# Performance work log

Measured on AMD Instinct MI355X. Metric: run time of the kernel, lower is better.

Reference implementation:

```python
import jax, jax.numpy as jnp
import numpy as np

N_LAGS = 64
EPS = 1e-8


def setup_inputs() -> dict:
    key = jax.random.key(0)
    x = jax.random.normal(key, (16, 8, 250, 1024), dtype=jnp.float32)
    return {"x": x}


def reference(x):
    B, M, T, L = x.shape
    # rfft over all mics once (shared across pairs)
    X = jnp.fft.rfft(x, axis=-1)  # [B, M, T, L//2+1] complex
    # all mic pairs (m1 < m2), row-major order matching the torch double loop
    i1, i2 = np.triu_indices(M, k=1)
    X1 = X[:, i1]  # [B, P, T, F]
    X2 = X[:, i2]  # [B, P, T, F]
    R = X1 * jnp.conj(X2)
    R = R / (jnp.abs(R) + EPS)  # PHAT weighting
    cc = jnp.fft.irfft(R, n=L, axis=-1)        # [B, P, T, L]
    cc = jnp.fft.fftshift(cc, axes=-1)
    center = L // 2
    start = center - N_LAGS // 2
    return cc[..., start:start + N_LAGS]        # [B, P, T, n_lags]
```

## Files before the change

### kernel.cpp

```cpp
#include <hip/hip_runtime.h>
#include <math.h>

#define B_    16
#define M_    8
#define T_    250
#define L_    1024
#define NPAIR 28

#define KTOT   1024
#define CH_K   256
#define APITCH 264
#define NKT    8
#define NCHUNK 4
#define ZPITCH 1056

typedef _Float16 half8  __attribute__((ext_vector_type(8)));
typedef _Float16 half2t __attribute__((ext_vector_type(2)));
typedef float    floatx4 __attribute__((ext_vector_type(4)));

__device__ __align__(16) _Float16 g_Btw[64 * KTOT];

__constant__ int c_i1[NPAIR] = {0,0,0,0,0,0,0,1,1,1,1,1,1,2,2,2,2,2,3,3,3,3,4,4,4,5,5,6};
__constant__ int c_i2[NPAIR] = {1,2,3,4,5,6,7,2,3,4,5,6,7,3,4,5,6,7,4,5,6,7,5,6,7,6,7,7};

__global__ void init_btw() {
    int idx = blockIdx.x * 256 + threadIdx.x;
    int n = idx >> 10, k = idx & 1023;
    float v;
    if (k == 0)      v = 1.0f / 1024.0f;
    else if (k == 1) v = (n & 1) ? (-1.0f / 1024.0f) : (1.0f / 1024.0f);
    else {
        int bin = k >> 1, tau = n - 32;
        int r = (tau * bin) & 1023;
        float ang = (float)r * (6.283185307179586f / 1024.0f);
        float s, c; sincosf(ang, &s, &c);
        v = ((k & 1) ? -s : c) * (2.0f / 1024.0f);
    }
    g_Btw[idx] = (_Float16)v;
}

#define SWZ(i) ((i) + ((i) >> 5))

__device__ inline float2 cmul(float2 a, float2 b) {
    return make_float2(fmaf(a.x, b.x, -a.y * b.y), fmaf(a.x, b.y, a.y * b.x));
}
__device__ inline float2 cadd(float2 a, float2 b) { return make_float2(a.x + b.x, a.y + b.y); }
__device__ inline float2 csub(float2 a, float2 b) { return make_float2(a.x - b.x, a.y - b.y); }
__device__ inline float2 cmni(float2 a) { return make_float2(a.y, -a.x); }

__device__ inline void dft8(float2 v[8]) {
    const float rt = 0.70710678118654752440f;
    float2 b0 = cadd(v[0], v[4]), b1 = cadd(v[1], v[5]);
    float2 b2 = cadd(v[2], v[6]), b3 = cadd(v[3], v[7]);
    float2 c0 = csub(v[0], v[4]);
    float2 t1 = csub(v[1], v[5]);
    float2 c1 = make_float2(rt * (t1.x + t1.y), rt * (t1.y - t1.x));
    float2 c2 = cmni(csub(v[2], v[6]));
    float2 t3 = csub(v[3], v[7]);
    float2 c3 = make_float2(rt * (t3.y - t3.x), -rt * (t3.x + t3.y));
    float2 f0 = cadd(b0, b2), f1 = cadd(b1, b3);
    float2 g0 = csub(b0, b2), g1 = cmni(csub(b1, b3));
    v[0] = cadd(f0, f1); v[4] = csub(f0, f1);
    v[2] = cadd(g0, g1); v[6] = csub(g0, g1);
    f0 = cadd(c0, c2); f1 = cadd(c1, c3);
    g0 = csub(c0, c2); g1 = cmni(csub(c1, c3));
    v[1] = cadd(f0, f1); v[5] = csub(f0, f1);
    v[3] = cadd(g0, g1); v[7] = csub(g0, g1);
}

__device__ inline void twiddle8(float2 v[8], float2 w1) {
    float2 w = w1;
    v[1] = cmul(v[1], w);
#pragma unroll
    for (int k = 2; k < 8; ++k) { w = cmul(w, w1); v[k] = cmul(v[k], w); }
}

__device__ inline int posmap(int k) {
    return ((k & 1) << 9) | (((k >> 1) & 7) << 6) | (((k >> 4) & 7) << 3) | ((k >> 7) & 7);
}

__global__ __launch_bounds__(512, 4) void gcc_main(const float* __restrict__ x,
                                                   float* __restrict__ out) {
    __shared__ float2 s_z[4 * ZPITCH];
    __shared__ __align__(16) union {
        float2   lut[512];
        _Float16 A[32 * APITCH];
    } su;

    const int tid = threadIdx.x;
    const int t = blockIdx.x, b = blockIdx.y;
    const int f = tid & 127, c = tid >> 7;
    float2* Zb = s_z + c * ZPITCH;

    {
        float s, cv, ang = (float)tid * (-6.283185307179586f / 1024.0f);
        sincosf(ang, &s, &cv);
        su.lut[tid] = make_float2(cv, s);
    }

    const float* xa = x + (((size_t)b * M_ + 2 * c) * T_ + t) * L_;
    const float* xb = xa + (size_t)T_ * L_;
#pragma unroll
    for (int e = 0; e < 2; ++e) {
        float4 va = *(const float4*)(xa + f * 8 + e * 4);
        float4 vb = *(const float4*)(xb + f * 8 + e * 4);
        int i = f * 8 + e * 4;
        Zb[SWZ(i + 0)] = make_float2(va.x, vb.x);
        Zb[SWZ(i + 1)] = make_float2(va.y, vb.y);
        Zb[SWZ(i + 2)] = make_float2(va.z, vb.z);
        Zb[SWZ(i + 3)] = make_float2(va.w, vb.w);
    }
    __syncthreads();

#pragma unroll
    for (int q = 0; q < 4; ++q) {
        int u = f + 128 * q;
        float2 a = Zb[SWZ(u)], d = Zb[SWZ(u + 512)];
        Zb[SWZ(u)]       = cadd(a, d);
        Zb[SWZ(u + 512)] = cmul(csub(a, d), su.lut[u]);
    }
    __syncthreads();

    {
        const int base = (f >> 6) * 512 + (f & 63);
        float2 v[8];
#pragma unroll
        for (int r = 0; r < 8; ++r) v[r] = Zb[SWZ(base + 64 * r)];
        dft8(v);
        twiddle8(v, su.lut[2 * (f & 63)]);
#pragma unroll
        for (int k = 0; k < 8; ++k) Zb[SWZ(base + 64 * k)] = v[k];
    }
    __syncthreads();

    {
        const int base = (f >> 3) * 64 + (f & 7);
        float2 v[8];
#pragma unroll
        for (int r = 0; r < 8; ++r) v[r] = Zb[SWZ(base + 8 * r)];
        dft8(v);
        twiddle8(v, su.lut[16 * (f & 7)]);
#pragma unroll
        for (int k = 0; k < 8; ++k) Zb[SWZ(base + 8 * k)] = v[k];
    }
    __syncthreads();

    {
        const int base = f * 8;
        float2 v[8];
#pragma unroll
        for (int r = 0; r < 8; ++r) v[r] = Zb[SWZ(base + r)];
        dft8(v);
#pragma unroll
        for (int k = 0; k < 8; ++k) Zb[SWZ(base + k)] = v[k];
    }
    __syncthreads();

    const int lane = tid & 63, wv = tid >> 6;
    const int mt = wv >> 2, nt = wv & 3;
    const int l15 = lane & 15, quad = lane >> 4;
    const int arow = mt * 16 + l15;
    const _Float16* Bbase = g_Btw + (nt * 16 + l15) * KTOT;
    floatx4 acc = {0.0f, 0.0f, 0.0f, 0.0f};

    const int bl = tid & 127, pg = tid >> 7;

#define PAIRA(p_, a_, b_)                                                     \
    {                                                                         \
        float2 X1 = Xs[a_], X2 = Xs[b_];                                      \
        float rr = X1.x * X2.x + X1.y * X2.y;                                 \
        float ri = X1.y * X2.x - X1.x * X2.y;                                 \
        float m2 = rr * rr + ri * ri;                                         \
        float inv = (m2 > 1e-30f) ? rsqrtf(m2) : 0.0f;                        \
        *(half2t*)&su.A[(p_) * APITCH + 2 * bl] =                             \
            (half2t){(_Float16)(rr * inv), (_Float16)(ri * inv)};             \
    }

    auto fillA = [&](int h) {
        const int beta = h * 128 + bl;
        const int pa = posmap(beta);
        const int pb = posmap((1024 - beta) & 1023);
        float2 Xs[8];
#pragma unroll
        for (int cc = 0; cc < 4; ++cc) {
            float2 Aa = s_z[cc * ZPITCH + SWZ(pa)];
            float2 Bb = s_z[cc * ZPITCH + SWZ(pb)];
            Xs[2 * cc]     = make_float2(0.5f * (Aa.x + Bb.x), 0.5f * (Aa.y - Bb.y));
            Xs[2 * cc + 1] = make_float2(0.5f * (Aa.y + Bb.y), 0.5f * (Bb.x - Aa.x));
        }
        if (pg == 0) {
            PAIRA(0, 0, 1) PAIRA(1, 0, 2) PAIRA(2, 0, 3) PAIRA(3, 0, 4)
            PAIRA(4, 0, 5) PAIRA(5, 0, 6) PAIRA(6, 0, 7)
        } else if (pg == 1) {
            PAIRA(7, 1, 2) PAIRA(8, 1, 3) PAIRA(9, 1, 4) PAIRA(10, 1, 5)
            PAIRA(11, 1, 6) PAIRA(12, 1, 7) PAIRA(13, 2, 3)
        } else if (pg == 2) {
            PAIRA(14, 2, 4) PAIRA(15, 2, 5) PAIRA(16, 2, 6) PAIRA(17, 2, 7)
            PAIRA(18, 3, 4) PAIRA(19, 3, 5) PAIRA(20, 3, 6)
        } else {
            PAIRA(21, 3, 7) PAIRA(22, 4, 5) PAIRA(23, 4, 6) PAIRA(24, 4, 7)
            PAIRA(25, 5, 6) PAIRA(26, 5, 7) PAIRA(27, 6, 7)
        }
        if (h == 0 && bl == 0) {
#pragma unroll
            for (int pp = 0; pp < 7; ++pp) {
                const int p = pg * 7 + pp;
                const int pN = posmap(512);
                float2 Za = s_z[(c_i1[p] >> 1) * ZPITCH + SWZ(pN)];
                float2 Zc = s_z[(c_i2[p] >> 1) * ZPITCH + SWZ(pN)];
                float x1 = (c_i1[p] & 1) ? Za.y : Za.x;
                float x2 = (c_i2[p] & 1) ? Zc.y : Zc.x;
                float rr = x1 * x2;
                float inv = (rr * rr > 1e-30f) ? rsqrtf(rr * rr) : 0.0f;
                su.A[p * APITCH + 1] = (_Float16)(rr * inv);
            }
        }
    };

    for (int h = 0; h < NCHUNK; ++h) {
        fillA(h);
        __syncthreads();

        const _Float16* Ap = su.A + arow * APITCH;
        const _Float16* Bp = Bbase + h * CH_K;
#pragma unroll
        for (int kt = 0; kt < NKT; ++kt) {
            half8 af = *(const half8*)(Ap + kt * 32 + quad * 8);
            half8 bf = *(const half8*)(Bp + kt * 32 + quad * 8);
            acc = __builtin_amdgcn_mfma_f32_16x16x32_f16(af, bf, acc, 0, 0, 0);
        }
        __syncthreads();
    }

#pragma unroll
    for (int r = 0; r < 4; ++r) {
        int pair = mt * 16 + quad * 4 + r;
        if (pair < NPAIR)
            out[((((size_t)b * NPAIR + pair) * T_ + t) << 6) + nt * 16 + l15] = acc[r];
    }
}

extern "C" void kernel_launch(void* const* d_in, const int* in_sizes, int n_in,
                              void* d_out, int out_size, void* d_ws, size_t ws_size,
                              hipStream_t stream) {
    (void)in_sizes; (void)n_in; (void)d_ws; (void)ws_size; (void)out_size;
    hipLaunchKernelGGL(init_btw, dim3(256), dim3(256), 0, stream);
    hipLaunchKernelGGL(gcc_main, dim3(T_, B_), dim3(512), 0, stream,
                       (const float*)d_in[0], (float*)d_out);
}
```

Measured before the change: 294.8 us.

## Cut LDS footprint with XOR swizzles, register twiddles, smaller A chunks

Replaces padded shared-memory layouts with XOR-swizzled unpadded ones and drops the twiddle lookup table, computing twiddles with sincosf in registers instead. The A staging buffer shrinks to 128-wide chunks (8 chunks of 4 MFMAs), and the pair-normalisation work is redistributed over all 8 waves. The first FFT stage is fused with the global load, using strided coalesced reads. Together these reduce LDS use so launch bounds can request 8 blocks per CU, at the cost of twice as many barriers in the MFMA loop and extra trig work per thread.

```diff
diff --git a/kernel.cpp b/kernel.cpp
--- a/kernel.cpp
+++ b/kernel.cpp
@@ -8,11 +8,9 @@
 #define NPAIR 28
 
 #define KTOT   1024
-#define CH_K   256
-#define APITCH 264
-#define NKT    8
-#define NCHUNK 4
-#define ZPITCH 1056
+#define CH_K   128
+#define NKT    4
+#define NCHUNK 8
 
 typedef _Float16 half8  __attribute__((ext_vector_type(8)));
 typedef _Float16 half2t __attribute__((ext_vector_type(2)));
@@ -39,7 +37,8 @@
     g_Btw[idx] = (_Float16)v;
 }
 
-#define SWZ(i) ((i) + ((i) >> 5))
+#define PHI(i) ((i) ^ (((i) >> 4) & 15) ^ ((((i) >> 8) & 3) << 1))
+#define AXR(p) (8 * ((p) & 7))
 
 __device__ inline float2 cmul(float2 a, float2 b) {
     return make_float2(fmaf(a.x, b.x, -a.y * b.y), fmaf(a.x, b.y, a.y * b.x));
@@ -79,69 +78,70 @@
     return ((k & 1) << 9) | (((k >> 1) & 7) << 6) | (((k >> 4) & 7) << 3) | ((k >> 7) & 7);
 }
 
-__global__ __launch_bounds__(512, 4) void gcc_main(const float* __restrict__ x,
+__global__ __launch_bounds__(512, 8) void gcc_main(const float* __restrict__ x,
                                                    float* __restrict__ out) {
-    __shared__ float2 s_z[4 * ZPITCH];
-    __shared__ __align__(16) union {
-        float2   lut[512];
-        _Float16 A[32 * APITCH];
-    } su;
+    __shared__ float2 s_z[4 * 1024];
+    __shared__ __align__(16) _Float16 sA[32 * CH_K];
 
     const int tid = threadIdx.x;
     const int t = blockIdx.x, b = blockIdx.y;
     const int f = tid & 127, c = tid >> 7;
-    float2* Zb = s_z + c * ZPITCH;
-
-    {
-        float s, cv, ang = (float)tid * (-6.283185307179586f / 1024.0f);
-        sincosf(ang, &s, &cv);
-        su.lut[tid] = make_float2(cv, s);
-    }
-
-    const float* xa = x + (((size_t)b * M_ + 2 * c) * T_ + t) * L_;
-    const float* xb = xa + (size_t)T_ * L_;
-#pragma unroll
-    for (int e = 0; e < 2; ++e) {
-        float4 va = *(const float4*)(xa + f * 8 + e * 4);
-        float4 vb = *(const float4*)(xb + f * 8 + e * 4);
-        int i = f * 8 + e * 4;
-        Zb[SWZ(i + 0)] = make_float2(va.x, vb.x);
-        Zb[SWZ(i + 1)] = make_float2(va.y, vb.y);
-        Zb[SWZ(i + 2)] = make_float2(va.z, vb.z);
-        Zb[SWZ(i + 3)] = make_float2(va.w, vb.w);
-    }
-    __syncthreads();
-
-#pragma unroll
-    for (int q = 0; q < 4; ++q) {
-        int u = f + 128 * q;
-        float2 a = Zb[SWZ(u)], d = Zb[SWZ(u + 512)];
-        Zb[SWZ(u)]       = cadd(a, d);
-        Zb[SWZ(u + 512)] = cmul(csub(a, d), su.lut[u]);
-    }
-    __syncthreads();
-
-    {
+    float2* Zb = s_z + c * 1024;
+
+    float ws, wc;
+    sincosf((float)f * (-6.283185307179586f / 1024.0f), &ws, &wc);
+    const float2 w = make_float2(wc, ws);
+
+    {
+        const float* xa = x + (((size_t)b * M_ + 2 * c) * T_ + t) * L_;
+        const float* xb = xa + (size_t)T_ * L_;
+        float va[8], vb[8];
+#pragma unroll
+        for (int j = 0; j < 8; ++j) { va[j] = xa[f + 128 * j]; vb[j] = xb[f + 128 * j]; }
+        const float rt = 0.70710678118654752440f;
+#pragma unroll
+        for (int q = 0; q < 4; ++q) {
+            float2 a = make_float2(va[q], vb[q]);
+            float2 d = make_float2(va[q + 4], vb[q + 4]);
+            float2 tq = cmul(csub(a, d), w);
+            float2 r;
+            if (q == 0)      r = tq;
+            else if (q == 1) r = make_float2(rt * (tq.x + tq.y), rt * (tq.y - tq.x));
+            else if (q == 2) r = make_float2(tq.y, -tq.x);
+            else             r = make_float2(rt * (tq.y - tq.x), -rt * (tq.x + tq.y));
+            Zb[PHI(f + 128 * q)]       = cadd(a, d);
+            Zb[PHI(f + 128 * q + 512)] = r;
+        }
+    }
+    __syncthreads();
+
+    {
+        float2 wl = w;
+        if (f & 64) wl = cmul(wl, make_float2(0.92387953251128674f, 0.38268343236508977f));
+        const float2 wB = cmul(wl, wl);
         const int base = (f >> 6) * 512 + (f & 63);
         float2 v[8];
 #pragma unroll
-        for (int r = 0; r < 8; ++r) v[r] = Zb[SWZ(base + 64 * r)];
+        for (int r = 0; r < 8; ++r) v[r] = Zb[PHI(base + 64 * r)];
         dft8(v);
-        twiddle8(v, su.lut[2 * (f & 63)]);
-#pragma unroll
-        for (int k = 0; k < 8; ++k) Zb[SWZ(base + 64 * k)] = v[k];
-    }
-    __syncthreads();
-
-    {
+        twiddle8(v, wB);
+#pragma unroll
+        for (int k = 0; k < 8; ++k) Zb[PHI(base + 64 * k)] = v[k];
+    }
+    __syncthreads();
+
+    {
+        float s2, c2;
+        sincosf((float)(f & 7) * (-6.283185307179586f / 64.0f), &s2, &c2);
+        const float2 wC = make_float2(c2, s2);
         const int base = (f >> 3) * 64 + (f & 7);
         float2 v[8];
 #pragma unroll
-        for (int r = 0; r < 8; ++r) v[r] = Zb[SWZ(base + 8 * r)];
+        for (int r = 0; r < 8; ++r) v[r] = Zb[PHI(base + 8 * r)];
         dft8(v);
-        twiddle8(v, su.lut[16 * (f & 7)]);
-#pragma unroll
-        for (int k = 0; k < 8; ++k) Zb[SWZ(base + 8 * k)] = v[k];
+        twiddle8(v, wC);
+#pragma unroll
+        for (int k = 0; k < 8; ++k) Zb[PHI(base + 8 * k)] = v[k];
     }
     __syncthreads();
 
@@ -149,10 +149,10 @@
         const int base = f * 8;
         float2 v[8];
 #pragma unroll
-        for (int r = 0; r < 8; ++r) v[r] = Zb[SWZ(base + r)];
+        for (int r = 0; r < 8; ++r) v[r] = Zb[PHI(base + r)];
         dft8(v);
 #pragma unroll
-        for (int k = 0; k < 8; ++k) Zb[SWZ(base + k)] = v[k];
+        for (int k = 0; k < 8; ++k) Zb[PHI(base + k)] = v[k];
     }
     __syncthreads();
 
@@ -163,7 +163,10 @@
     const _Float16* Bbase = g_Btw + (nt * 16 + l15) * KTOT;
     floatx4 acc = {0.0f, 0.0f, 0.0f, 0.0f};
 
-    const int bl = tid & 127, pg = tid >> 7;
+    const int bl = lane;
+    const int pg = wv;
+
+    if (tid < 256) ((unsigned int*)sA)[1792 + tid] = 0u;
 
 #define PAIRA(p_, a_, b_)                                                     \
     {                                                                         \
@@ -172,47 +175,53 @@
         float ri = X1.y * X2.x - X1.x * X2.y;                                 \
         float m2 = rr * rr + ri * ri;                                         \
         float inv = (m2 > 1e-30f) ? rsqrtf(m2) : 0.0f;                        \
-        *(half2t*)&su.A[(p_) * APITCH + 2 * bl] =                             \
+        *(half2t*)&sA[(p_) * CH_K + ((2 * bl) ^ AXR(p_))] =                   \
             (half2t){(_Float16)(rr * inv), (_Float16)(ri * inv)};             \
     }
 
     auto fillA = [&](int h) {
-        const int beta = h * 128 + bl;
+        const int beta = h * 64 + bl;
         const int pa = posmap(beta);
         const int pb = posmap((1024 - beta) & 1023);
         float2 Xs[8];
 #pragma unroll
         for (int cc = 0; cc < 4; ++cc) {
-            float2 Aa = s_z[cc * ZPITCH + SWZ(pa)];
-            float2 Bb = s_z[cc * ZPITCH + SWZ(pb)];
+            float2 Aa = s_z[cc * 1024 + PHI(pa)];
+            float2 Bb = s_z[cc * 1024 + PHI(pb)];
             Xs[2 * cc]     = make_float2(0.5f * (Aa.x + Bb.x), 0.5f * (Aa.y - Bb.y));
             Xs[2 * cc + 1] = make_float2(0.5f * (Aa.y + Bb.y), 0.5f * (Bb.x - Aa.x));
         }
         if (pg == 0) {
             PAIRA(0, 0, 1) PAIRA(1, 0, 2) PAIRA(2, 0, 3) PAIRA(3, 0, 4)
-            PAIRA(4, 0, 5) PAIRA(5, 0, 6) PAIRA(6, 0, 7)
         } else if (pg == 1) {
-            PAIRA(7, 1, 2) PAIRA(8, 1, 3) PAIRA(9, 1, 4) PAIRA(10, 1, 5)
-            PAIRA(11, 1, 6) PAIRA(12, 1, 7) PAIRA(13, 2, 3)
+            PAIRA(4, 0, 5) PAIRA(5, 0, 6) PAIRA(6, 0, 7) PAIRA(7, 1, 2)
         } else if (pg == 2) {
-            PAIRA(14, 2, 4) PAIRA(15, 2, 5) PAIRA(16, 2, 6) PAIRA(17, 2, 7)
-            PAIRA(18, 3, 4) PAIRA(19, 3, 5) PAIRA(20, 3, 6)
+            PAIRA(8, 1, 3) PAIRA(9, 1, 4) PAIRA(10, 1, 5) PAIRA(11, 1, 6)
+        } else if (pg == 3) {
+            PAIRA(12, 1, 7) PAIRA(13, 2, 3) PAIRA(14, 2, 4) PAIRA(15, 2, 5)
+        } else if (pg == 4) {
+            PAIRA(16, 2, 6) PAIRA(17, 2, 7) PAIRA(18, 3, 4)
+        } else if (pg == 5) {
+            PAIRA(19, 3, 5) PAIRA(20, 3, 6) PAIRA(21, 3, 7)
+        } else if (pg == 6) {
+            PAIRA(22, 4, 5) PAIRA(23, 4, 6) PAIRA(24, 4, 7)
         } else {
-            PAIRA(21, 3, 7) PAIRA(22, 4, 5) PAIRA(23, 4, 6) PAIRA(24, 4, 7)
             PAIRA(25, 5, 6) PAIRA(26, 5, 7) PAIRA(27, 6, 7)
         }
         if (h == 0 && bl == 0) {
-#pragma unroll
-            for (int pp = 0; pp < 7; ++pp) {
-                const int p = pg * 7 + pp;
-                const int pN = posmap(512);
-                float2 Za = s_z[(c_i1[p] >> 1) * ZPITCH + SWZ(pN)];
-                float2 Zc = s_z[(c_i2[p] >> 1) * ZPITCH + SWZ(pN)];
+            const int p0 = (pg < 4) ? 4 * pg : 16 + 3 * (pg - 4);
+            const int cnt = (pg < 4) ? 4 : 3;
+            const int pN = 4;
+#pragma unroll
+            for (int pp = 0; pp < cnt; ++pp) {
+                const int p = p0 + pp;
+                float2 Za = s_z[(c_i1[p] >> 1) * 1024 + pN];
+                float2 Zc = s_z[(c_i2[p] >> 1) * 1024 + pN];
                 float x1 = (c_i1[p] & 1) ? Za.y : Za.x;
                 float x2 = (c_i2[p] & 1) ? Zc.y : Zc.x;
                 float rr = x1 * x2;
                 float inv = (rr * rr > 1e-30f) ? rsqrtf(rr * rr) : 0.0f;
-                su.A[p * APITCH + 1] = (_Float16)(rr * inv);
+                sA[p * CH_K + (1 ^ AXR(p))] = (_Float16)(rr * inv);
             }
         }
     };
@@ -221,11 +230,11 @@
         fillA(h);
         __syncthreads();
 
-        const _Float16* Ap = su.A + arow * APITCH;
         const _Float16* Bp = Bbase + h * CH_K;
+        const int ax = AXR(arow);
 #pragma unroll
         for (int kt = 0; kt < NKT; ++kt) {
-            half8 af = *(const half8*)(Ap + kt * 32 + quad * 8);
+            half8 af = *(const half8*)(sA + arow * CH_K + ((kt * 32 + quad * 8) ^ ax));
             half8 bf = *(const half8*)(Bp + kt * 32 + quad * 8);
             acc = __builtin_amdgcn_mfma_f32_16x16x32_f16(af, bf, acc, 0, 0, 0);
         }
```

Result: slower. 320.6 us (+8.8%).
